# Optimization experiments

Measured on AMD Instinct MI355X. Metric: run time of the kernel, lower is better.

Reference implementation:

```python
import jax, jax.numpy as jnp
import numpy as np

N = 50000   # nodes
E = 800000  # edges
IN, HID, OUT = 128, 128, 64


def setup_inputs() -> dict:
    key = jax.random.key(0)
    ks = jax.random.split(key, 16)
    x = jax.random.normal(ks[0], (N, IN), dtype=jnp.float32)
    src = jax.random.randint(ks[1], (E,), 0, N, dtype=jnp.int32)
    dst = jax.random.randint(ks[2], (E,), 0, N, dtype=jnp.int32)
    s = 1.0 / np.sqrt(IN)
    W_self1 = jax.random.normal(ks[3], (IN, HID), dtype=jnp.float32) * s
    W_neigh1 = jax.random.normal(ks[4], (IN, HID), dtype=jnp.float32) * s
    b1 = jnp.zeros((HID,), dtype=jnp.float32)
    W_self2 = jax.random.normal(ks[5], (HID, HID), dtype=jnp.float32) * s
    W_neigh2 = jax.random.normal(ks[6], (HID, HID), dtype=jnp.float32) * s
    b2 = jnp.zeros((HID,), dtype=jnp.float32)
    W_self3 = jax.random.normal(ks[7], (HID, OUT), dtype=jnp.float32) * s
    W_neigh3 = jax.random.normal(ks[8], (HID, OUT), dtype=jnp.float32) * s
    b3 = jnp.zeros((OUT,), dtype=jnp.float32)
    # dropout(p=0.5) masks, pre-scaled by 1/(1-p)
    keep = 0.5
    mask1 = (jax.random.uniform(ks[9], (N, HID)) < keep).astype(jnp.float32) / keep
    mask2 = (jax.random.uniform(ks[10], (N, HID)) < keep).astype(jnp.float32) / keep
    return dict(x=x, src=src, dst=dst,
                W_self1=W_self1, W_neigh1=W_neigh1, b1=b1,
                W_self2=W_self2, W_neigh2=W_neigh2, b2=b2,
                W_self3=W_self3, W_neigh3=W_neigh3, b3=b3,
                mask1=mask1, mask2=mask2)


def _mean_agg(h, src, dst):
    # gather source features, segment-sum into destinations, divide by in-degree
    summed = jax.ops.segment_sum(h[src], dst, num_segments=N)  # [N, d]
    deg = jax.ops.segment_sum(jnp.ones((E,), dtype=h.dtype), dst, num_segments=N)
    return summed / jnp.maximum(deg, 1.0)[:, None]


def _sage_layer(h, src, dst, W_self, W_neigh, b):
    h_neigh = _mean_agg(h, src, dst)
    return h @ W_self + h_neigh @ W_neigh + b


def reference(x, src, dst, W_self1, W_neigh1, b1, W_self2, W_neigh2, b2,
              W_self3, W_neigh3, b3, mask1, mask2):
    h = _sage_layer(x, src, dst, W_self1, W_neigh1, b1)
    h = jax.nn.relu(h) * mask1
    h = _sage_layer(h, src, dst, W_self2, W_neigh2, b2)
    h = jax.nn.relu(h) * mask2
    h = _sage_layer(h, src, dst, W_self3, W_neigh3, b3)
    return h
```

## Files before the change

### kernel.cpp

```cpp
#include <hip/hip_runtime.h>
#include <hip/hip_bf16.h>

#define DIN  128
#define DHID 128
#define DOUT 64

#define EB   4096
#define CAPB 5120

typedef short short8 __attribute__((ext_vector_type(8)));
typedef float f32x4  __attribute__((ext_vector_type(4)));

__device__ __forceinline__ ushort f2bf(float f) {
    union { float f; uint u; } c; c.f = f;
    uint u = c.u;
    return (ushort)((u + 0x7fff + ((u >> 16) & 1)) >> 16);
}
__device__ __forceinline__ float bf2f(uint h16) {
    union { uint u; float f; } c; c.u = h16 << 16;
    return c.f;
}
__device__ __forceinline__ float sb8(uint u, int k) {
    return (float)((int)(u << (24 - 8 * k)) >> 24);
}

__device__ __forceinline__ void wprep_dev(const float* __restrict__ W,
                                          ushort* __restrict__ Wt, int OUT, int idx) {
    int nn = idx >> 7;
    int k  = idx & 127;
    Wt[idx] = f2bf(W[(size_t)k * OUT + nn]);
}

__global__ __launch_bounds__(256)
void megaprep(const int* __restrict__ src, const int* __restrict__ dst, int E, int fillB,
              int* __restrict__ bkt_cur, uint* __restrict__ pairs,
              const float* __restrict__ x, ushort* __restrict__ xb, int n4, int cvtB,
              const float* __restrict__ Ws1, const float* __restrict__ Wn1,
              const float* __restrict__ Ws2, const float* __restrict__ Wn2,
              const float* __restrict__ Ws3, const float* __restrict__ Wn3,
              ushort* __restrict__ Wst1, ushort* __restrict__ Wnt1,
              ushort* __restrict__ Wst2, ushort* __restrict__ Wnt2,
              ushort* __restrict__ Wst3, ushort* __restrict__ Wnt3) {
    __shared__ int c[256];
    __shared__ int startl[256];
    __shared__ int ofs[256];
    int b = blockIdx.x;
    const int t = threadIdx.x;
    if (b < fillB) {
        c[t] = 0;
        __syncthreads();
        const int base = b * EB;
        const int end = min(base + EB, E);
        for (int i = base + t; i < end; i += 256)
            atomicAdd(&c[dst[i] >> 8], 1);
        __syncthreads();
        int v = c[t];
        startl[t] = v ? (t * CAPB + atomicAdd(&bkt_cur[t], v)) : 0;
        ofs[t] = 0;
        __syncthreads();
        for (int i = base + t; i < end; i += 256) {
            int d = dst[i];
            int bb = d >> 8;
            int p = startl[bb] + atomicAdd(&ofs[bb], 1);
            pairs[p] = ((uint)src[i] << 8) | (uint)(d & 255);
        }
        return;
    }
    b -= fillB;
    if (b < cvtB) {
        int i = b * 256 + t;
        if (i < n4) {
            float4 v = ((const float4*)x)[i];
            ushort4 o;
            o.x = f2bf(v.x); o.y = f2bf(v.y); o.z = f2bf(v.z); o.w = f2bf(v.w);
            ((ushort4*)xb)[i] = o;
        }
        return;
    }
    b -= cvtB;
    if (b < 64)  { wprep_dev(Ws1, Wst1, 128, b * 256 + t); return; }
    b -= 64;
    if (b < 64)  { wprep_dev(Wn1, Wnt1, 128, b * 256 + t); return; }
    b -= 64;
    if (b < 64)  { wprep_dev(Ws2, Wst2, 128, b * 256 + t); return; }
    b -= 64;
    if (b < 64)  { wprep_dev(Wn2, Wnt2, 128, b * 256 + t); return; }
    b -= 64;
    if (b < 32)  { wprep_dev(Ws3, Wst3, 64, b * 256 + t); return; }
    b -= 32;
    wprep_dev(Wn3, Wnt3, 64, b * 256 + t);
}

__global__ __launch_bounds__(256)
void bucket_csr(const uint* __restrict__ pairs, const int* __restrict__ bkt_cur,
                int* __restrict__ row_ptr, int* __restrict__ deg,
                int* __restrict__ esrc, int N, int nbkt) {
    constexpr int CAP = 6144;
    __shared__ uint pl[CAP];
    __shared__ int cnt[256];
    __shared__ int rs[256];
    __shared__ int sc[256];
    const int bkt = blockIdx.x;
    const int t = threadIdx.x;
    const int ebase = bkt * CAPB;
    const int ecnt  = min(bkt_cur[bkt], CAPB);
    cnt[t] = 0;
    __syncthreads();
    const bool fits = (ecnt <= CAP);
    if (fits) {
        for (int i = t; i < ecnt; i += 256) {
            uint p = pairs[ebase + i];
            pl[i] = p;
            atomicAdd(&cnt[p & 255u], 1);
        }
    } else {
        for (int i = t; i < ecnt; i += 256)
            atomicAdd(&cnt[pairs[ebase + i] & 255u], 1);
    }
    __syncthreads();
    int own = cnt[t];
    sc[t] = own;
    __syncthreads();
    for (int o = 1; o < 256; o <<= 1) {
        int u = (t >= o) ? sc[t - o] : 0;
        __syncthreads();
        sc[t] += u;
        __syncthreads();
    }
    rs[t] = sc[t] - own;
    const int node = bkt * 256 + t;
    if (node < N) {
        row_ptr[node] = ebase + rs[t];
        deg[node] = own;
    }
    __syncthreads();
    if (fits) {
        for (int i = t; i < ecnt; i += 256) {
            uint p = pl[i];
            int pos = atomicAdd(&rs[p & 255u], 1);
            esrc[ebase + pos] = (int)(p >> 8);
        }
    } else {
        for (int i = t; i < ecnt; i += 256) {
            uint p = pairs[ebase + i];
            int pos = atomicAdd(&rs[p & 255u], 1);
            esrc[ebase + pos] = (int)(p >> 8);
        }
    }
}

template<int OUTW>
__global__ __launch_bounds__(256)
void sage_gemm(const ushort* __restrict__ Hb,
               const ushort* __restrict__ Wst,
               const ushort* __restrict__ Wnt,
               ushort* __restrict__ S,
               signed char* __restrict__ Gq,
               float* __restrict__ Gsc,
               int n) {
    constexpr int NT = OUTW / 16;
    __shared__ ushort Wl[2][OUTW * 128];

    const int tid  = threadIdx.x;
    const int lane = tid & 63;
    const int wave = tid >> 6;
    const int rg   = wave >> 1;
    const int isG  = wave & 1;
    const int m16  = lane & 15;
    const int kb   = lane >> 4;
    const int rbase = blockIdx.x * 64 + rg * 32;

    {
        const uint4* s4 = (const uint4*)Wst;
        const uint4* n4 = (const uint4*)Wnt;
        uint4* ls = (uint4*)&Wl[0][0];
        uint4* ln = (uint4*)&Wl[1][0];
#pragma unroll
        for (int j = tid; j < OUTW * 128 / 8; j += 256) {
            ls[j] = s4[j];
            ln[j] = n4[j];
        }
    }

    short8 a[2][4];
#pragma unroll
    for (int mt = 0; mt < 2; ++mt) {
        int arow = rbase + mt * 16 + m16;
        if (arow >= n) arow = n - 1;
        const ushort* __restrict__ Ap = &Hb[(size_t)arow * 128 + kb * 8];
#pragma unroll
        for (int c = 0; c < 4; ++c)
            a[mt][c] = *(const short8*)(Ap + c * 32);
    }

    __syncthreads();

    f32x4 acc[2][NT];
#pragma unroll
    for (int mt = 0; mt < 2; ++mt)
#pragma unroll
        for (int t = 0; t < NT; ++t) acc[mt][t] = (f32x4)(0.f);

    const ushort* __restrict__ Wp = &Wl[isG][0];
#pragma unroll
    for (int t = 0; t < NT; ++t) {
#pragma unroll
        for (int c = 0; c < 4; ++c) {
            short8 b = *(const short8*)&Wp[(t * 16 + m16) * 128 + c * 32 + kb * 8];
            acc[0][t] = __builtin_amdgcn_mfma_f32_16x16x32_bf16(a[0][c], b, acc[0][t], 0, 0, 0);
            acc[1][t] = __builtin_amdgcn_mfma_f32_16x16x32_bf16(a[1][c], b, acc[1][t], 0, 0, 0);
        }
    }

#pragma unroll
    for (int mt = 0; mt < 2; ++mt) {
        const int rb = rbase + mt * 16;
        if (!isG) {
#pragma unroll
            for (int r = 0; r < 4; ++r) {
                int row = rb + kb * 4 + r;
                if (row >= n) continue;
#pragma unroll
                for (int t = 0; t < NT; ++t)
                    S[(size_t)row * OUTW + t * 16 + m16] = f2bf(acc[mt][t][r]);
            }
        } else {
#pragma unroll
            for (int r = 0; r < 4; ++r) {
                float mx = 0.f;
#pragma unroll
                for (int t = 0; t < NT; ++t) mx = fmaxf(mx, fabsf(acc[mt][t][r]));
                mx = fmaxf(mx, __shfl_xor(mx, 1));
                mx = fmaxf(mx, __shfl_xor(mx, 2));
                mx = fmaxf(mx, __shfl_xor(mx, 4));
                mx = fmaxf(mx, __shfl_xor(mx, 8));
                int row = rb + kb * 4 + r;
                if (row >= n) continue;
                float inv = (mx > 0.f) ? 127.f / mx : 0.f;
                if (m16 == 0) Gsc[row] = mx * (1.f / 127.f);
#pragma unroll
                for (int t = 0; t < NT; ++t) {
                    int q = (int)rintf(acc[mt][t][r] * inv);
                    q = max(-127, min(127, q));
                    Gq[(size_t)row * OUTW + t * 16 + m16] = (signed char)q;
                }
            }
        }
    }
}

__device__ __forceinline__ void acc8(float* af, uint2 v, float sc) {
    af[0] += sc * sb8(v.x, 0); af[1] += sc * sb8(v.x, 1);
    af[2] += sc * sb8(v.x, 2); af[3] += sc * sb8(v.x, 3);
    af[4] += sc * sb8(v.y, 0); af[5] += sc * sb8(v.y, 1);
    af[6] += sc * sb8(v.y, 2); af[7] += sc * sb8(v.y, 3);
}
__device__ __forceinline__ void acc16(float* af, uint4 v, float sc) {
    af[0]  += sc * sb8(v.x, 0); af[1]  += sc * sb8(v.x, 1);
    af[2]  += sc * sb8(v.x, 2); af[3]  += sc * sb8(v.x, 3);
    af[4]  += sc * sb8(v.y, 0); af[5]  += sc * sb8(v.y, 1);
    af[6]  += sc * sb8(v.y, 2); af[7]  += sc * sb8(v.y, 3);
    af[8]  += sc * sb8(v.z, 0); af[9]  += sc * sb8(v.z, 1);
    af[10] += sc * sb8(v.z, 2); af[11] += sc * sb8(v.z, 3);
    af[12] += sc * sb8(v.w, 0); af[13] += sc * sb8(v.w, 1);
    af[14] += sc * sb8(v.w, 2); af[15] += sc * sb8(v.w, 3);
}

#define WCAP 320

#define LOADW16(V, C, base_)                                        \
    _Pragma("unroll")                                               \
    for (int k = 0; k < 4; ++k) {                                   \
        uint2 p = iw[(base_) + k];                                  \
        V[k] = *(const uint4*)&gp[(size_t)p.x * 128];               \
        C[k] = __uint_as_float(p.y);                                \
    }
#define LOADW8(V, C, base_)                                         \
    _Pragma("unroll")                                               \
    for (int k = 0; k < 4; ++k) {                                   \
        uint2 p = iw[(base_) + k];                                  \
        V[k] = *(const uint2*)&gp[(size_t)p.x * 64];                \
        C[k] = __uint_as_float(p.y);                                \
    }
#define CONSW16(V, C)                                               \
    _Pragma("unroll") for (int k = 0; k < 4; ++k) acc16(af, V[k], C[k]);
#define CONSW8(V, C)                                                \
    _Pragma("unroll") for (int k = 0; k < 4; ++k) acc8(af, V[k], C[k]);

template<bool FINAL>
__global__ __launch_bounds__(128)
void sage_gather(const signed char* __restrict__ Gq, const float* __restrict__ Gsc,
                 const ushort* __restrict__ S, const float* __restrict__ bias,
                 const float* __restrict__ mask,
                 const int* __restrict__ row_ptr, const int* __restrict__ deg,
                 const int* __restrict__ esrc,
                 void* __restrict__ outv, int n) {
    __shared__ uint2 is_s[2][WCAP];

    const int tid  = threadIdx.x;
    const int wave = tid >> 6;
    const int lane = tid & 63;
    const int g    = lane >> 3;
    const int l8   = lane & 7;
    const int wbase = blockIdx.x * 16 + wave * 8;
    if (wbase >= n) return;

    const int node = wbase + g;
    int d = 0, rp = 0;
    if (node < n) { d = deg[node]; rp = row_ptr[node]; }

    const int last   = min(wbase + 7, n - 1);
    const int span_s = row_ptr[wbase];
    const int span_e = row_ptr[last] + deg[last];
    const int len    = span_e - span_s;
    uint2* __restrict__ iw = is_s[wave];
    const bool staged = (len <= WCAP);
    if (staged) {
        int sA[5];
#pragma unroll
        for (int r = 0; r < 5; ++r) {
            int i = lane + r * 64;
            sA[r] = (i < len) ? esrc[span_s + i] : 0;
        }
#pragma unroll
        for (int r = 0; r < 5; ++r) {
            int i = lane + r * 64;
            if (i < len)
                iw[i] = make_uint2((uint)sA[r], __float_as_uint(Gsc[sA[r]]));
        }
    }

    if (node >= n) return;
    const float inv = 1.f / fmaxf((float)d, 1.f);

    if (!FINAL) {
        float af[16];
#pragma unroll
        for (int q = 0; q < 16; ++q) af[q] = 0.f;
        const signed char* __restrict__ gp = Gq + l8 * 16;
        const int col0 = l8 * 16;

        if (staged) {
            int i = rp - span_s;
            const int e = i + d;
            const int nf = d >> 2;
            uint4 vA[4], vB[4]; float cA[4], cB[4];
            if (nf >= 1) { LOADW16(vA, cA, i); }
            if (nf >= 2) { LOADW16(vB, cB, i + 4); }
            int b = 0;
            for (; b + 2 <= nf; b += 2) {
                CONSW16(vA, cA);
                if (b + 2 < nf) { LOADW16(vA, cA, i + 8); }
                CONSW16(vB, cB);
                if (b + 3 < nf) { LOADW16(vB, cB, i + 12); }
                i += 8;
            }
            if (b < nf) { CONSW16(vA, cA); i += 4; }
            for (; i < e; ++i) {
                uint2 p = iw[i];
                acc16(af, *(const uint4*)&gp[(size_t)p.x * 128], __uint_as_float(p.y));
            }
        } else {
            int i = rp, e = i + d;
            for (; i < e; ++i) {
                int ns = esrc[i];
                acc16(af, *(const uint4*)&gp[(size_t)ns * 128], Gsc[ns]);
            }
        }
        uint4 sa = *(const uint4*)&S[(size_t)node * 128 + col0];
        uint4 sb = *(const uint4*)&S[(size_t)node * 128 + col0 + 8];
        float bv[16], mv[16];
#pragma unroll
        for (int q = 0; q < 4; ++q) {
            *(float4*)&bv[q * 4] = *(const float4*)&bias[col0 + q * 4];
            *(float4*)&mv[q * 4] = *(const float4*)&mask[(size_t)node * 128 + col0 + q * 4];
        }
        uint sv[8] = {sa.x, sa.y, sa.z, sa.w, sb.x, sb.y, sb.z, sb.w};
        uint pk[8];
#pragma unroll
        for (int q = 0; q < 8; ++q) {
            float z0 = bf2f(sv[q] & 0xffffu) + af[2 * q]     * inv + bv[2 * q];
            float z1 = bf2f(sv[q] >> 16)     + af[2 * q + 1] * inv + bv[2 * q + 1];
            z0 = fmaxf(z0, 0.f) * mv[2 * q];
            z1 = fmaxf(z1, 0.f) * mv[2 * q + 1];
            pk[q] = (uint)f2bf(z0) | ((uint)f2bf(z1) << 16);
        }
        ushort* op = (ushort*)outv + (size_t)node * 128 + col0;
        uint4 o0, o1;
        o0.x = pk[0]; o0.y = pk[1]; o0.z = pk[2]; o0.w = pk[3];
        o1.x = pk[4]; o1.y = pk[5]; o1.z = pk[6]; o1.w = pk[7];
        *(uint4*)op = o0;
        *(uint4*)(op + 8) = o1;
    } else {
        float af[8];
#pragma unroll
        for (int q = 0; q < 8; ++q) af[q] = 0.f;
        const signed char* __restrict__ gp = Gq + l8 * 8;
        const int col0 = l8 * 8;

        if (staged) {
            int i = rp - span_s;
            const int e = i + d;
            const int nf = d >> 2;
            uint2 vA[4], vB[4]; float cA[4], cB[4];
            if (nf >= 1) { LOADW8(vA, cA, i); }
            if (nf >= 2) { LOADW8(vB, cB, i + 4); }
            int b = 0;
            for (; b + 2 <= nf; b += 2) {
                CONSW8(vA, cA);
                if (b + 2 < nf) { LOADW8(vA, cA, i + 8); }
                CONSW8(vB, cB);
                if (b + 3 < nf) { LOADW8(vB, cB, i + 12); }
                i += 8;
            }
            if (b < nf) { CONSW8(vA, cA); i += 4; }
            for (; i < e; ++i) {
                uint2 p = iw[i];
                acc8(af, *(const uint2*)&gp[(size_t)p.x * 64], __uint_as_float(p.y));
            }
        } else {
            int i = rp, e = i + d;
            for (; i < e; ++i) {
                int ns = esrc[i];
                acc8(af, *(const uint2*)&gp[(size_t)ns * 64], Gsc[ns]);
            }
        }
        uint4 sv4 = *(const uint4*)&S[(size_t)node * 64 + col0];
        float bv[8];
        *(float4*)&bv[0] = *(const float4*)&bias[col0];
        *(float4*)&bv[4] = *(const float4*)&bias[col0 + 4];
        uint sv[4] = {sv4.x, sv4.y, sv4.z, sv4.w};
        float z[8];
#pragma unroll
        for (int q = 0; q < 4; ++q) {
            z[2 * q]     = bf2f(sv[q] & 0xffffu) + af[2 * q]     * inv + bv[2 * q];
            z[2 * q + 1] = bf2f(sv[q] >> 16)     + af[2 * q + 1] * inv + bv[2 * q + 1];
        }
        float* op = (float*)outv + (size_t)node * 64 + col0;
        float4 o0, o1;
        o0.x = z[0]; o0.y = z[1]; o0.z = z[2]; o0.w = z[3];
        o1.x = z[4]; o1.y = z[5]; o1.z = z[6]; o1.w = z[7];
        *(float4*)&op[0] = o0;
        *(float4*)&op[4] = o1;
    }
}

extern "C" void kernel_launch(void* const* d_in, const int* in_sizes, int n_in,
                              void* d_out, int out_size, void* d_ws, size_t ws_size,
                              hipStream_t stream) {
    const float* x   = (const float*)d_in[0];
    const int*   src = (const int*)d_in[1];
    const int*   dst = (const int*)d_in[2];
    const float* Ws1 = (const float*)d_in[3];
    const float* Wn1 = (const float*)d_in[4];
    const float* b1  = (const float*)d_in[5];
    const float* Ws2 = (const float*)d_in[6];
    const float* Wn2 = (const float*)d_in[7];
    const float* b2  = (const float*)d_in[8];
    const float* Ws3 = (const float*)d_in[9];
    const float* Wn3 = (const float*)d_in[10];
    const float* b3  = (const float*)d_in[11];
    const float* mask1 = (const float*)d_in[12];
    const float* mask2 = (const float*)d_in[13];
    float* out = (float*)d_out;

    const int N = in_sizes[0] / DIN;
    const int E = in_sizes[1];
    const int nbkt = (N + 255) >> 8;

    char* ws = (char*)d_ws;
    int* bkt_cur  = (int*)ws;
    int* row_ptr  = bkt_cur + 256;
    int* deg      = row_ptr + N;
    int* esrc     = deg + N;
    size_t off = ((size_t)(256 + 2 * N + nbkt * CAPB) * sizeof(int) + 255) & ~(size_t)255;
    uint* pairs  = (uint*)(ws + off);    off += (size_t)nbkt * CAPB * 4;
    ushort* xb   = (ushort*)(ws + off);  off += (size_t)N * 128 * 2;
    ushort* h1b  = (ushort*)(ws + off);  off += (size_t)N * 128 * 2;
    ushort* h2b  = (ushort*)(ws + off);  off += (size_t)N * 128 * 2;
    ushort* S    = (ushort*)(ws + off);  off += (size_t)N * 128 * 2;
    signed char* Gq = (signed char*)(ws + off); off += (size_t)N * 128;
    float* Gsc   = (float*)(ws + off);   off += (size_t)N * 4;
    ushort* Wst1 = (ushort*)(ws + off);  off += 128 * 128 * 2;
    ushort* Wnt1 = (ushort*)(ws + off);  off += 128 * 128 * 2;
    ushort* Wst2 = (ushort*)(ws + off);  off += 128 * 128 * 2;
    ushort* Wnt2 = (ushort*)(ws + off);  off += 128 * 128 * 2;
    ushort* Wst3 = (ushort*)(ws + off);  off += 64 * 128 * 2;
    ushort* Wnt3 = (ushort*)(ws + off);  off += 64 * 128 * 2;

    const int n4 = N * 128 / 4;
    const int cvtB = (n4 + 255) / 256;
    const int fillB = (E + EB - 1) / EB;

    hipMemsetAsync(bkt_cur, 0, 256 * sizeof(int), stream);
    megaprep<<<fillB + cvtB + 4 * 64 + 2 * 32, 256, 0, stream>>>(
        src, dst, E, fillB, bkt_cur, pairs,
        x, xb, n4, cvtB,
        Ws1, Wn1, Ws2, Wn2, Ws3, Wn3,
        Wst1, Wnt1, Wst2, Wnt2, Wst3, Wnt3);

    bucket_csr<<<nbkt, 256, 0, stream>>>(pairs, bkt_cur, row_ptr, deg, esrc, N, nbkt);

    const int gemmB = (N + 63) / 64;
    const int gathB = (N + 15) / 16;

    sage_gemm<128><<<gemmB, 256, 0, stream>>>(xb, Wst1, Wnt1, S, Gq, Gsc, N);
    sage_gather<false><<<gathB, 128, 0, stream>>>(Gq, Gsc, S, b1, mask1, row_ptr, deg, esrc, h1b, N);
    sage_gemm<128><<<gemmB, 256, 0, stream>>>(h1b, Wst2, Wnt2, S, Gq, Gsc, N);
    sage_gather<false><<<gathB, 128, 0, stream>>>(Gq, Gsc, S, b2, mask2, row_ptr, deg, esrc, h2b, N);
    sage_gemm<64><<<gemmB, 256, 0, stream>>>(h2b, Wst3, Wnt3, S, Gq, Gsc, N);
    sage_gather<true><<<gathB, 128, 0, stream>>>(Gq, Gsc, S, b3, nullptr, row_ptr, deg, esrc, out, N);
}
```

Before: 284.3 us.

## Replace bucketed CSR build with global degree count, scan, and atomic scatter

Replaces the two-pass bucketed pair sort (shared-memory bucket histograms, capacity-bounded buckets, per-bucket CSR) with a plain CSR build. The new build does a global atomic degree count, a two-level exclusive scan (local scan plus a single-block fold) and an atomic-cursor scatter of source ids. This removes the bucket capacity limits and the packed pairs buffer, but adds global atomics on node counters, two extra kernel launches and a serial single-block fold over all nodes. The gather loop also now pads its tail with masked loads instead of a scalar remainder loop, and the self-term S load is hoisted ahead of the neighbour accumulation.

```diff
diff --git a/kernel.cpp b/kernel.cpp
--- a/kernel.cpp
+++ b/kernel.cpp
@@ -5,8 +5,8 @@
 #define DHID 128
 #define DOUT 64
 
-#define EB   4096
-#define CAPB 5120
+#define CNTB 392
+#define SCTB 392
 
 typedef short short8 __attribute__((ext_vector_type(8)));
 typedef float f32x4  __attribute__((ext_vector_type(4)));
@@ -32,8 +32,8 @@
 }
 
 __global__ __launch_bounds__(256)
-void megaprep(const int* __restrict__ src, const int* __restrict__ dst, int E, int fillB,
-              int* __restrict__ bkt_cur, uint* __restrict__ pairs,
+void megaprep(const int* __restrict__ dst, int E,
+              int* __restrict__ deg,
               const float* __restrict__ x, ushort* __restrict__ xb, int n4, int cvtB,
               const float* __restrict__ Ws1, const float* __restrict__ Wn1,
               const float* __restrict__ Ws2, const float* __restrict__ Wn2,
@@ -41,32 +41,15 @@
               ushort* __restrict__ Wst1, ushort* __restrict__ Wnt1,
               ushort* __restrict__ Wst2, ushort* __restrict__ Wnt2,
               ushort* __restrict__ Wst3, ushort* __restrict__ Wnt3) {
-    __shared__ int c[256];
-    __shared__ int startl[256];
-    __shared__ int ofs[256];
     int b = blockIdx.x;
     const int t = threadIdx.x;
-    if (b < fillB) {
-        c[t] = 0;
-        __syncthreads();
-        const int base = b * EB;
-        const int end = min(base + EB, E);
-        for (int i = base + t; i < end; i += 256)
-            atomicAdd(&c[dst[i] >> 8], 1);
-        __syncthreads();
-        int v = c[t];
-        startl[t] = v ? (t * CAPB + atomicAdd(&bkt_cur[t], v)) : 0;
-        ofs[t] = 0;
-        __syncthreads();
-        for (int i = base + t; i < end; i += 256) {
-            int d = dst[i];
-            int bb = d >> 8;
-            int p = startl[bb] + atomicAdd(&ofs[bb], 1);
-            pairs[p] = ((uint)src[i] << 8) | (uint)(d & 255);
-        }
+    if (b < CNTB) {
+        const int stride = CNTB * 256;
+        for (int i = b * 256 + t; i < E; i += stride)
+            atomicAdd(&deg[dst[i]], 1);
         return;
     }
-    b -= fillB;
+    b -= CNTB;
     if (b < cvtB) {
         int i = b * 256 + t;
         if (i < n4) {
@@ -92,33 +75,13 @@
 }
 
 __global__ __launch_bounds__(256)
-void bucket_csr(const uint* __restrict__ pairs, const int* __restrict__ bkt_cur,
-                int* __restrict__ row_ptr, int* __restrict__ deg,
-                int* __restrict__ esrc, int N, int nbkt) {
-    constexpr int CAP = 6144;
-    __shared__ uint pl[CAP];
-    __shared__ int cnt[256];
-    __shared__ int rs[256];
+void scan_local(const int* __restrict__ deg, int* __restrict__ row_ptr,
+                int* __restrict__ bsum, int N) {
     __shared__ int sc[256];
-    const int bkt = blockIdx.x;
+    const int b = blockIdx.x;
     const int t = threadIdx.x;
-    const int ebase = bkt * CAPB;
-    const int ecnt  = min(bkt_cur[bkt], CAPB);
-    cnt[t] = 0;
-    __syncthreads();
-    const bool fits = (ecnt <= CAP);
-    if (fits) {
-        for (int i = t; i < ecnt; i += 256) {
-            uint p = pairs[ebase + i];
-            pl[i] = p;
-            atomicAdd(&cnt[p & 255u], 1);
-        }
-    } else {
-        for (int i = t; i < ecnt; i += 256)
-            atomicAdd(&cnt[pairs[ebase + i] & 255u], 1);
-    }
-    __syncthreads();
-    int own = cnt[t];
+    const int node = b * 256 + t;
+    const int own = (node < N) ? deg[node] : 0;
     sc[t] = own;
     __syncthreads();
     for (int o = 1; o < 256; o <<= 1) {
@@ -127,25 +90,45 @@
         sc[t] += u;
         __syncthreads();
     }
-    rs[t] = sc[t] - own;
-    const int node = bkt * 256 + t;
-    if (node < N) {
-        row_ptr[node] = ebase + rs[t];
-        deg[node] = own;
-    }
+    if (node < N) row_ptr[node] = sc[t] - own;
+    if (t == 255) bsum[b] = sc[255];
+}
+
+__global__ __launch_bounds__(256)
+void scan_fold(int* __restrict__ row_ptr, int* __restrict__ cur,
+               const int* __restrict__ bsum, int N, int nblk) {
+    __shared__ int sc[256];
+    __shared__ int bo[256];
+    const int t = threadIdx.x;
+    const int v = (t < nblk) ? bsum[t] : 0;
+    sc[t] = v;
     __syncthreads();
-    if (fits) {
-        for (int i = t; i < ecnt; i += 256) {
-            uint p = pl[i];
-            int pos = atomicAdd(&rs[p & 255u], 1);
-            esrc[ebase + pos] = (int)(p >> 8);
-        }
-    } else {
-        for (int i = t; i < ecnt; i += 256) {
-            uint p = pairs[ebase + i];
-            int pos = atomicAdd(&rs[p & 255u], 1);
-            esrc[ebase + pos] = (int)(p >> 8);
-        }
+    for (int o = 1; o < 256; o <<= 1) {
+        int u = (t >= o) ? sc[t - o] : 0;
+        __syncthreads();
+        sc[t] += u;
+        __syncthreads();
+    }
+    bo[t] = sc[t] - v;
+    __syncthreads();
+    for (int base = 0; base < N; base += 256) {
+        const int node = base + t;
+        if (node < N) {
+            int r = row_ptr[node] + bo[node >> 8];
+            row_ptr[node] = r;
+            cur[node] = r;
+        }
+    }
+}
+
+__global__ __launch_bounds__(256)
+void scatter_csr(const int* __restrict__ src, const int* __restrict__ dst,
+                 int* __restrict__ cur, int* __restrict__ esrc, int E) {
+    const int t = blockIdx.x * 256 + threadIdx.x;
+    const int stride = SCTB * 256;
+    for (int i = t; i < E; i += stride) {
+        int p = atomicAdd(&cur[dst[i]], 1);
+        esrc[p] = src[i];
     }
 }
 
@@ -268,23 +251,27 @@
 
 #define WCAP 320
 
-#define LOADW16(V, C, base_)                                        \
+#define LOADT16(V, C, j_)                                           \
     _Pragma("unroll")                                               \
     for (int k = 0; k < 4; ++k) {                                   \
-        uint2 p = iw[(base_) + k];                                  \
-        V[k] = *(const uint4*)&gp[(size_t)p.x * 128];               \
-        C[k] = __uint_as_float(p.y);                                \
-    }
-#define LOADW8(V, C, base_)                                         \
+        int p_ = i0 + (j_) * 4 + k;                                 \
+        bool ok_ = p_ < e_;                                         \
+        uint2 pr_ = iw[ok_ ? p_ : i0];                              \
+        V[k] = *(const uint4*)&gp[(size_t)pr_.x * 128];             \
+        C[k] = ok_ ? __uint_as_float(pr_.y) : 0.f;                  \
+    }
+#define LOADT8(V, C, j_)                                            \
     _Pragma("unroll")                                               \
     for (int k = 0; k < 4; ++k) {                                   \
-        uint2 p = iw[(base_) + k];                                  \
-        V[k] = *(const uint2*)&gp[(size_t)p.x * 64];                \
-        C[k] = __uint_as_float(p.y);                                \
-    }
-#define CONSW16(V, C)                                               \
+        int p_ = i0 + (j_) * 4 + k;                                 \
+        bool ok_ = p_ < e_;                                         \
+        uint2 pr_ = iw[ok_ ? p_ : i0];                              \
+        V[k] = *(const uint2*)&gp[(size_t)pr_.x * 64];              \
+        C[k] = ok_ ? __uint_as_float(pr_.y) : 0.f;                  \
+    }
+#define CONST16(V, C)                                               \
     _Pragma("unroll") for (int k = 0; k < 4; ++k) acc16(af, V[k], C[k]);
-#define CONSW8(V, C)                                                \
+#define CONST8(V, C)                                                \
     _Pragma("unroll") for (int k = 0; k < 4; ++k) acc8(af, V[k], C[k]);
 
 template<bool FINAL>
@@ -339,26 +326,26 @@
         for (int q = 0; q < 16; ++q) af[q] = 0.f;
         const signed char* __restrict__ gp = Gq + l8 * 16;
         const int col0 = l8 * 16;
+        uint4 sa = *(const uint4*)&S[(size_t)node * 128 + col0];
+        uint4 sb = *(const uint4*)&S[(size_t)node * 128 + col0 + 8];
 
         if (staged) {
-            int i = rp - span_s;
-            const int e = i + d;
-            const int nf = d >> 2;
+            const int i0 = rp - span_s;
+            const int e_ = i0 + d;
+            const int nb = (d + 3) >> 2;
             uint4 vA[4], vB[4]; float cA[4], cB[4];
-            if (nf >= 1) { LOADW16(vA, cA, i); }
-            if (nf >= 2) { LOADW16(vB, cB, i + 4); }
-            int b = 0;
-            for (; b + 2 <= nf; b += 2) {
-                CONSW16(vA, cA);
-                if (b + 2 < nf) { LOADW16(vA, cA, i + 8); }
-                CONSW16(vB, cB);
-                if (b + 3 < nf) { LOADW16(vB, cB, i + 12); }
-                i += 8;
-            }
-            if (b < nf) { CONSW16(vA, cA); i += 4; }
-            for (; i < e; ++i) {
-                uint2 p = iw[i];
-                acc16(af, *(const uint4*)&gp[(size_t)p.x * 128], __uint_as_float(p.y));
+            if (nb > 0) {
+                LOADT16(vA, cA, 0);
+                if (nb > 1) { LOADT16(vB, cB, 1); }
+                int b = 0;
+                while (true) {
+                    CONST16(vA, cA);
+                    if (b + 2 < nb) { LOADT16(vA, cA, b + 2); }
+                    ++b; if (b >= nb) break;
+                    CONST16(vB, cB);
+                    if (b + 2 < nb) { LOADT16(vB, cB, b + 2); }
+                    ++b; if (b >= nb) break;
+                }
             }
         } else {
             int i = rp, e = i + d;
@@ -367,8 +354,6 @@
                 acc16(af, *(const uint4*)&gp[(size_t)ns * 128], Gsc[ns]);
             }
         }
-        uint4 sa = *(const uint4*)&S[(size_t)node * 128 + col0];
-        uint4 sb = *(const uint4*)&S[(size_t)node * 128 + col0 + 8];
         float bv[16], mv[16];
 #pragma unroll
         for (int q = 0; q < 4; ++q) {
@@ -397,26 +382,25 @@
         for (int q = 0; q < 8; ++q) af[q] = 0.f;
         const signed char* __restrict__ gp = Gq + l8 * 8;
         const int col0 = l8 * 8;
+        uint4 sv4 = *(const uint4*)&S[(size_t)node * 64 + col0];
 
         if (staged) {
-            int i = rp - span_s;
-            const int e = i + d;
-            const int nf = d >> 2;
+            const int i0 = rp - span_s;
+            const int e_ = i0 + d;
+            const int nb = (d + 3) >> 2;
             uint2 vA[4], vB[4]; float cA[4], cB[4];
-            if (nf >= 1) { LOADW8(vA, cA, i); }
-            if (nf >= 2) { LOADW8(vB, cB, i + 4); }
-            int b = 0;
-            for (; b + 2 <= nf; b += 2) {
-                CONSW8(vA, cA);
-                if (b + 2 < nf) { LOADW8(vA, cA, i + 8); }
-                CONSW8(vB, cB);
-                if (b + 3 < nf) { LOADW8(vB, cB, i + 12); }
-                i += 8;
-            }
-            if (b < nf) { CONSW8(vA, cA); i += 4; }
-            for (; i < e; ++i) {
-                uint2 p = iw[i];
-                acc8(af, *(const uint2*)&gp[(size_t)p.x * 64], __uint_as_float(p.y));
+            if (nb > 0) {
+                LOADT8(vA, cA, 0);
+                if (nb > 1) { LOADT8(vB, cB, 1); }
+                int b = 0;
+                while (true) {
+                    CONST8(vA, cA);
+                    if (b + 2 < nb) { LOADT8(vA, cA, b + 2); }
+                    ++b; if (b >= nb) break;
+                    CONST8(vB, cB);
+                    if (b + 2 < nb) { LOADT8(vB, cB, b + 2); }
+                    ++b; if (b >= nb) break;
+                }
             }
         } else {
             int i = rp, e = i + d;
@@ -425,7 +409,6 @@
                 acc8(af, *(const uint2*)&gp[(size_t)ns * 64], Gsc[ns]);
             }
         }
-        uint4 sv4 = *(const uint4*)&S[(size_t)node * 64 + col0];
         float bv[8];
         *(float4*)&bv[0] = *(const float4*)&bias[col0];
         *(float4*)&bv[4] = *(const float4*)&bias[col0 + 4];
@@ -466,15 +449,15 @@
 
     const int N = in_sizes[0] / DIN;
     const int E = in_sizes[1];
-    const int nbkt = (N + 255) >> 8;
+    const int nblk = (N + 255) >> 8;
 
     char* ws = (char*)d_ws;
-    int* bkt_cur  = (int*)ws;
-    int* row_ptr  = bkt_cur + 256;
-    int* deg      = row_ptr + N;
-    int* esrc     = deg + N;
-    size_t off = ((size_t)(256 + 2 * N + nbkt * CAPB) * sizeof(int) + 255) & ~(size_t)255;
-    uint* pairs  = (uint*)(ws + off);    off += (size_t)nbkt * CAPB * 4;
+    int* row_ptr = (int*)ws;
+    int* deg     = row_ptr + N;
+    int* cur     = deg + N;
+    int* bsum    = cur + N;
+    int* esrc    = bsum + 256;
+    size_t off = ((size_t)(3 * N + 256 + E) * sizeof(int) + 255) & ~(size_t)255;
     ushort* xb   = (ushort*)(ws + off);  off += (size_t)N * 128 * 2;
     ushort* h1b  = (ushort*)(ws + off);  off += (size_t)N * 128 * 2;
     ushort* h2b  = (ushort*)(ws + off);  off += (size_t)N * 128 * 2;
@@ -490,16 +473,16 @@
 
     const int n4 = N * 128 / 4;
     const int cvtB = (n4 + 255) / 256;
-    const int fillB = (E + EB - 1) / EB;
-
-    hipMemsetAsync(bkt_cur, 0, 256 * sizeof(int), stream);
-    megaprep<<<fillB + cvtB + 4 * 64 + 2 * 32, 256, 0, stream>>>(
-        src, dst, E, fillB, bkt_cur, pairs,
+
+    hipMemsetAsync(deg, 0, (size_t)N * sizeof(int), stream);
+    megaprep<<<CNTB + cvtB + 4 * 64 + 2 * 32, 256, 0, stream>>>(
+        dst, E, deg,
         x, xb, n4, cvtB,
         Ws1, Wn1, Ws2, Wn2, Ws3, Wn3,
         Wst1, Wnt1, Wst2, Wnt2, Wst3, Wnt3);
-
-    bucket_csr<<<nbkt, 256, 0, stream>>>(pairs, bkt_cur, row_ptr, deg, esrc, N, nbkt);
+    scan_local<<<nblk, 256, 0, stream>>>(deg, row_ptr, bsum, N);
+    scan_fold<<<1, 256, 0, stream>>>(row_ptr, cur, bsum, N, nblk);
+    scatter_csr<<<SCTB, 256, 0, stream>>>(src, dst, cur, esrc, E);
 
     const int gemmB = (N + 63) / 64;
     const int gathB = (N + 15) / 16;
```

Result: slower. 387.2 us (+36.2%).
